# Optimization experiments

Hardware: AMD Instinct MI355X
Metric: run time of the kernel (lower is better)

Reference implementation:

```python
import jax, jax.numpy as jnp
import numpy as np
from jax import lax

M, B, D = 32, 64, 8192  # history length, batch of systems, degrees of freedom


def setup_inputs() -> dict:
    key = jax.random.key(0)
    k1, k2, k3 = jax.random.split(key, 3)
    s = jax.random.normal(k1, (M, B, D), dtype=jnp.float32)
    y = jax.random.normal(k2, (M, B, D), dtype=jnp.float32)
    frc = jax.random.normal(k3, (B, D), dtype=jnp.float32)
    return {"s": s, "y": y, "frc": frc}


def reference(s, y, frc):
    # r_i = 1 / (s_i . y_i), per batch row, as stored by extend()
    r = 1.0 / jnp.sum(s * y, axis=-1, keepdims=True)  # [M, B, 1]

    # First loop: iterate history from newest (i = M-1) to oldest (i = 0)
    def back_step(q, carry):
        si, yi, ri = carry
        ai = ri * jnp.sum(si * q, axis=-1, keepdims=True)  # [B, 1]
        q = q - ai * yi
        return q, ai

    q0 = -frc
    q, a_rev = lax.scan(back_step, q0, (s[::-1], y[::-1], r[::-1]))
    a = a_rev[::-1]  # a[i] now aligned with history index i

    # Initial Hessian scaling gamma = (s_last . y_last) / (y_last . y_last)
    g = (jnp.sum(s[-1] * y[-1], axis=-1) / jnp.sum(y[-1] * y[-1], axis=-1))[:, None]
    q = g * q

    # Second loop: oldest to newest
    def fwd_step(q, carry):
        si, yi, ri, ai = carry
        bi = ri * jnp.sum(yi * q, axis=-1, keepdims=True)
        q = q + si * (ai - bi)
        return q, None

    q, _ = lax.scan(fwd_step, q, (s, y, r, a))
    return -q
```

## Files before the change

### kernel.cpp

```cpp
#include <hip/hip_runtime.h>

#define Mh 32
#define Bh 64
#define Dh 8192
#define KCH 1024
#define NCH (Dh / KCH)
#define STG 128
#define NST (KCH / STG)

#define OFF_PSY 0
#define OFF_PYY 524288
#define OFF_PVS 1048576
#define OFF_PVY (OFF_PVS + 16384)
#define OFF_CY  (OFF_PVY + 16384)
#define OFF_CS  (OFF_CY + 2048)
#define OFF_G   (OFF_CS + 2048)

__global__ __launch_bounds__(256) void gram_kernel(
    const float* __restrict__ s, const float* __restrict__ y,
    const float* __restrict__ frc, float* __restrict__ ws)
{
    __shared__ float sT[32 * STG];
    __shared__ float yT[32 * STG];
    __shared__ float fT[STG];

    const int b  = blockIdx.x & 63;
    const int ch = blockIdx.x >> 6;
    const int k0 = ch * KCH;
    const int t  = threadIdx.x;
    const int w  = t >> 6;
    const int l  = t & 63;
    const int tx = l & 7;
    const int ty = l >> 3;
    const size_t base = (size_t)b * Dh;

    float asy[4][4] = {};
    float ayy[4][4] = {};
    float avs[4] = {}, avy[4] = {};

    int ri[4], rc[4];
    #pragma unroll
    for (int rep = 0; rep < 4; ++rep) {
        const int idx = t + rep * 256;
        ri[rep] = idx >> 5;
        rc[rep] = idx & 31;
    }

    float4 pS[4], pY[4], pF;
    auto issue = [&](int kb) {
        #pragma unroll
        for (int rep = 0; rep < 4; ++rep) {
            const size_t off = ((size_t)ri[rep] * Bh) * Dh + base + kb + (rc[rep] << 2);
            pS[rep] = *(const float4*)(s + off);
            pY[rep] = *(const float4*)(y + off);
        }
        if (t < 32) pF = *(const float4*)(frc + base + kb + (t << 2));
    };

    issue(k0);
    for (int st = 0; st < NST; ++st) {
        __syncthreads();
        #pragma unroll
        for (int rep = 0; rep < 4; ++rep) {
            const int col = rc[rep] ^ ((ri[rep] >> 2) & 7);
            *(float4*)&sT[ri[rep] * STG + (col << 2)] = pS[rep];
            *(float4*)&yT[ri[rep] * STG + (col << 2)] = pY[rep];
        }
        if (t < 32) *(float4*)&fT[t << 2] = pF;
        __syncthreads();
        if (st + 1 < NST) issue(k0 + (st + 1) * STG);

        #pragma unroll
        for (int kk = 0; kk < 8; ++kk) {
            const int c0 = (w << 3) + kk;
            float4 sv[4], tv[4], xv[4];
            #pragma unroll
            for (int aa = 0; aa < 4; ++aa) {
                sv[aa] = *(const float4*)&sT[((ty << 2) + aa) * STG + ((c0 ^ ty) << 2)];
                tv[aa] = *(const float4*)&yT[((ty << 2) + aa) * STG + ((c0 ^ ty) << 2)];
                xv[aa] = *(const float4*)&yT[((tx << 2) + aa) * STG + ((c0 ^ tx) << 2)];
            }
            const float4 fv = *(const float4*)&fT[c0 << 2];
            #pragma unroll
            for (int aa = 0; aa < 4; ++aa) {
                #pragma unroll
                for (int cc = 0; cc < 4; ++cc) {
                    asy[aa][cc] += sv[aa].x * xv[cc].x + sv[aa].y * xv[cc].y
                                 + sv[aa].z * xv[cc].z + sv[aa].w * xv[cc].w;
                    ayy[aa][cc] += tv[aa].x * xv[cc].x + tv[aa].y * xv[cc].y
                                 + tv[aa].z * xv[cc].z + tv[aa].w * xv[cc].w;
                }
                avs[aa] += sv[aa].x * fv.x + sv[aa].y * fv.y + sv[aa].z * fv.z + sv[aa].w * fv.w;
                avy[aa] += tv[aa].x * fv.x + tv[aa].y * fv.y + tv[aa].z * fv.z + tv[aa].w * fv.w;
            }
        }
    }

    __syncthreads();
    for (int wv = 0; wv < 4; ++wv) {
        if (w == wv) {
            #pragma unroll
            for (int aa = 0; aa < 4; ++aa) {
                #pragma unroll
                for (int cc = 0; cc < 4; ++cc) {
                    const int e = ((ty << 2) + aa) * 32 + (tx << 2) + cc;
                    if (wv == 0) { sT[e] = asy[aa][cc];  yT[e] = ayy[aa][cc]; }
                    else         { sT[e] += asy[aa][cc]; yT[e] += ayy[aa][cc]; }
                }
                if (tx == 0) {
                    const int i = (ty << 2) + aa;
                    if (wv == 0) { fT[i] = avs[aa];  fT[32 + i] = avy[aa]; }
                    else         { fT[i] += avs[aa]; fT[32 + i] += avy[aa]; }
                }
            }
        }
        __syncthreads();
    }

    float* PSY = ws + OFF_PSY + ((size_t)ch * Bh + b) * 1024;
    float* PYY = ws + OFF_PYY + ((size_t)ch * Bh + b) * 1024;
    *(float4*)&PSY[t << 2] = *(const float4*)&sT[t << 2];
    *(float4*)&PYY[t << 2] = *(const float4*)&yT[t << 2];
    if (t < 32)      ws[OFF_PVS + (ch * 64 + b) * 32 + t] = fT[t];
    else if (t < 64) ws[OFF_PVY + (ch * 64 + b) * 32 + (t - 32)] = fT[t];
}

__global__ __launch_bounds__(256) void recur_kernel(float* __restrict__ ws)
{
    __shared__ float WSY[1024], WYY[1024], VS[32], VY[32];
    const int b = blockIdx.x;
    const int t = threadIdx.x;

    float4 a4 = make_float4(0.f, 0.f, 0.f, 0.f);
    float4 c4 = make_float4(0.f, 0.f, 0.f, 0.f);
    #pragma unroll
    for (int ch = 0; ch < NCH; ++ch) {
        const float4 u = *(const float4*)&ws[OFF_PSY + ((size_t)ch * Bh + b) * 1024 + (t << 2)];
        const float4 v = *(const float4*)&ws[OFF_PYY + ((size_t)ch * Bh + b) * 1024 + (t << 2)];
        a4.x += u.x; a4.y += u.y; a4.z += u.z; a4.w += u.w;
        c4.x += v.x; c4.y += v.y; c4.z += v.z; c4.w += v.w;
    }
    *(float4*)&WSY[t << 2] = a4;
    *(float4*)&WYY[t << 2] = c4;
    if (t < 32) {
        float av = 0.f, cv = 0.f;
        #pragma unroll
        for (int ch = 0; ch < NCH; ++ch) {
            av += ws[OFF_PVS + (ch * 64 + b) * 32 + t];
            cv += ws[OFF_PVY + (ch * 64 + b) * 32 + t];
        }
        VS[t] = av; VY[t] = cv;
    }
    __syncthreads();
    if (t >= 64) return;

    const int i = t & 31;
    float row_sy[32], col_sy[32], row_yy[32];
    #pragma unroll
    for (int j = 0; j < 32; ++j) {
        row_sy[j] = WSY[i * 32 + j];
        col_sy[j] = WSY[j * 32 + i];
        row_yy[j] = WYY[i * 32 + j];
    }

    const double r = 1.0 / (double)row_sy[i];
    double acc = -(double)VS[i];
    double a_val = 0.0;
    #pragma unroll
    for (int j = 31; j >= 0; --j) {
        const double aj = __shfl(r, j) * __shfl(acc, j);
        if (i == j) a_val = aj;
        if (i < j)  acc -= aj * (double)row_sy[j];
    }

    const double g = (double)WSY[31 * 32 + 31] / (double)WYY[31 * 32 + 31];

    double u = -(double)VY[i];
    #pragma unroll
    for (int j = 0; j < 32; ++j)
        u -= __shfl(a_val, j) * (double)row_yy[j];
    u *= g;

    double tt = u;
    double b_val = 0.0;
    #pragma unroll
    for (int j = 0; j < 32; ++j) {
        const double bj = __shfl(r, j) * __shfl(tt, j);
        if (i == j) b_val = bj;
        const double dj = __shfl(a_val, j) - bj;
        if (i > j) tt += dj * (double)col_sy[j];
    }

    if (t < 32) {
        ws[OFF_CY + b * 32 + i] = (float)(g * a_val);
        ws[OFF_CS + b * 32 + i] = (float)(b_val - a_val);
    }
    if (t == 0) ws[OFF_G + b] = (float)g;
}

__global__ __launch_bounds__(256) void combine_kernel(
    const float* __restrict__ s, const float* __restrict__ y,
    const float* __restrict__ frc, const float* __restrict__ ws,
    float* __restrict__ out)
{
    __shared__ float cy[32], cs[32];
    const int b  = blockIdx.x & 63;
    const int ch = blockIdx.x >> 6;
    const int t  = threadIdx.x;
    if (t < 32) { cy[t] = ws[OFF_CY + b * 32 + t]; cs[t] = ws[OFF_CS + b * 32 + t]; }
    __syncthreads();

    const int d = ch * 1024 + (t << 2);
    const size_t base = (size_t)b * Dh + d;
    const float g = ws[OFF_G + b];
    const float4 fv = *(const float4*)(frc + base);
    float4 acc;
    acc.x = g * fv.x; acc.y = g * fv.y; acc.z = g * fv.z; acc.w = g * fv.w;

    const float* py = y + base;
    const float* ps = s + base;
    #pragma unroll
    for (int grp = 0; grp < 4; ++grp) {
        float4 yv[8], sv[8];
        #pragma unroll
        for (int j = 0; j < 8; ++j) {
            const size_t off = (size_t)(grp * 8 + j) * ((size_t)Bh * Dh);
            yv[j] = *(const float4*)(py + off);
            sv[j] = *(const float4*)(ps + off);
        }
        #pragma unroll
        for (int j = 0; j < 8; ++j) {
            const float a1 = cy[grp * 8 + j], a2 = cs[grp * 8 + j];
            acc.x += a1 * yv[j].x + a2 * sv[j].x;
            acc.y += a1 * yv[j].y + a2 * sv[j].y;
            acc.z += a1 * yv[j].z + a2 * sv[j].z;
            acc.w += a1 * yv[j].w + a2 * sv[j].w;
        }
    }
    *(float4*)(out + base) = acc;
}

extern "C" void kernel_launch(void* const* d_in, const int* in_sizes, int n_in,
                              void* d_out, int out_size, void* d_ws, size_t ws_size,
                              hipStream_t stream)
{
    const float* s   = (const float*)d_in[0];
    const float* y   = (const float*)d_in[1];
    const float* frc = (const float*)d_in[2];
    float* out = (float*)d_out;
    float* ws  = (float*)d_ws;

    gram_kernel<<<dim3(Bh * NCH), dim3(256), 0, stream>>>(s, y, frc, ws);
    recur_kernel<<<dim3(Bh), dim3(256), 0, stream>>>(ws);
    combine_kernel<<<dim3(Bh * NCH), dim3(256), 0, stream>>>(s, y, frc, ws, out);
}
```

Measured before the change: 255.7 us.

## Use async global-to-LDS loads in gram kernel and split combine into two passes

The gram kernel now streams s/y tiles directly into double-buffered LDS with global_load_lds and reads frc straight from global memory. The chunk count grows to 16 when the workspace allows, which doubles the number of gram blocks. The combine step optionally becomes two kernels: one writes per-history-row weighted rows to the workspace and another reduces them. That second path adds roughly 64MB of extra write and read traffic in exchange for more parallelism. Workspace offsets are now computed at runtime from ws_size.

```diff
diff --git a/kernel.cpp b/kernel.cpp
--- a/kernel.cpp
+++ b/kernel.cpp
@@ -3,92 +3,98 @@
 #define Mh 32
 #define Bh 64
 #define Dh 8192
-#define KCH 1024
-#define NCH (Dh / KCH)
 #define STG 128
-#define NST (KCH / STG)
-
-#define OFF_PSY 0
-#define OFF_PYY 524288
-#define OFF_PVS 1048576
-#define OFF_PVY (OFF_PVS + 16384)
-#define OFF_CY  (OFF_PVY + 16384)
-#define OFF_CS  (OFF_CY + 2048)
-#define OFF_G   (OFF_CS + 2048)
+
+typedef unsigned int u32;
+
+__device__ __forceinline__ void async_cp16(const float* g, float* l) {
+    __builtin_amdgcn_global_load_lds((const __attribute__((address_space(1))) u32*)g,
+                                     (__attribute__((address_space(3))) u32*)l, 16, 0, 0);
+}
 
 __global__ __launch_bounds__(256) void gram_kernel(
     const float* __restrict__ s, const float* __restrict__ y,
-    const float* __restrict__ frc, float* __restrict__ ws)
-{
-    __shared__ float sT[32 * STG];
-    __shared__ float yT[32 * STG];
-    __shared__ float fT[STG];
-
+    const float* __restrict__ frc, float* __restrict__ ws,
+    int nch, int kch,
+    long off_psy, long off_pyy, long off_pvs, long off_pvy)
+{
+    __shared__ float sT[2][32 * STG];
+    __shared__ float yT[2][32 * STG];
     const int b  = blockIdx.x & 63;
     const int ch = blockIdx.x >> 6;
-    const int k0 = ch * KCH;
+    const int k0 = ch * kch;
+    const int nst = kch / STG;
     const int t  = threadIdx.x;
     const int w  = t >> 6;
     const int l  = t & 63;
     const int tx = l & 7;
     const int ty = l >> 3;
-    const size_t base = (size_t)b * Dh;
-
-    float asy[4][4] = {};
-    float ayy[4][4] = {};
+
+    const float* sp[4]; const float* yp[4]; int lofs[4];
+    #pragma unroll
+    for (int jj = 0; jj < 4; ++jj) {
+        const int j   = (w << 2) + jj;
+        const int row = (j << 1) + (l >> 5);
+        const int cg  = (l & 31) ^ ((j >> 1) & 7);
+        const size_t goff = ((size_t)row * Bh + b) * Dh + k0 + (cg << 2);
+        sp[jj] = s + goff;
+        yp[jj] = y + goff;
+        lofs[jj] = j << 8;
+    }
+    const float* frcp = frc + (size_t)b * Dh + k0;
+
+    float acc_sy[4][4] = {};
+    float acc_yy[4][4] = {};
     float avs[4] = {}, avy[4] = {};
 
-    int ri[4], rc[4];
-    #pragma unroll
-    for (int rep = 0; rep < 4; ++rep) {
-        const int idx = t + rep * 256;
-        ri[rep] = idx >> 5;
-        rc[rep] = idx & 31;
-    }
-
-    float4 pS[4], pY[4], pF;
-    auto issue = [&](int kb) {
-        #pragma unroll
-        for (int rep = 0; rep < 4; ++rep) {
-            const size_t off = ((size_t)ri[rep] * Bh) * Dh + base + kb + (rc[rep] << 2);
-            pS[rep] = *(const float4*)(s + off);
-            pY[rep] = *(const float4*)(y + off);
-        }
-        if (t < 32) pF = *(const float4*)(frc + base + kb + (t << 2));
-    };
-
-    issue(k0);
-    for (int st = 0; st < NST; ++st) {
+    #pragma unroll
+    for (int jj = 0; jj < 4; ++jj) {
+        async_cp16(sp[jj], &sT[0][lofs[jj]]);
+        async_cp16(yp[jj], &yT[0][lofs[jj]]);
+        sp[jj] += STG; yp[jj] += STG;
+    }
+
+    for (int st = 0; st < nst; ++st) {
+        const int cur = st & 1;
         __syncthreads();
-        #pragma unroll
-        for (int rep = 0; rep < 4; ++rep) {
-            const int col = rc[rep] ^ ((ri[rep] >> 2) & 7);
-            *(float4*)&sT[ri[rep] * STG + (col << 2)] = pS[rep];
-            *(float4*)&yT[ri[rep] * STG + (col << 2)] = pY[rep];
-        }
-        if (t < 32) *(float4*)&fT[t << 2] = pF;
-        __syncthreads();
-        if (st + 1 < NST) issue(k0 + (st + 1) * STG);
-
+
+        float4 fvs[8];
+        #pragma unroll
+        for (int kk = 0; kk < 8; ++kk)
+            fvs[kk] = *(const float4*)(frcp + (((w << 3) + kk) << 2));
+        __builtin_amdgcn_sched_barrier(0);
+        frcp += STG;
+
+        if (st + 1 < nst) {
+            #pragma unroll
+            for (int jj = 0; jj < 4; ++jj) {
+                async_cp16(sp[jj], &sT[cur ^ 1][lofs[jj]]);
+                async_cp16(yp[jj], &yT[cur ^ 1][lofs[jj]]);
+                sp[jj] += STG; yp[jj] += STG;
+            }
+        }
+
+        const float* sb = sT[cur];
+        const float* yb = yT[cur];
         #pragma unroll
         for (int kk = 0; kk < 8; ++kk) {
             const int c0 = (w << 3) + kk;
             float4 sv[4], tv[4], xv[4];
             #pragma unroll
             for (int aa = 0; aa < 4; ++aa) {
-                sv[aa] = *(const float4*)&sT[((ty << 2) + aa) * STG + ((c0 ^ ty) << 2)];
-                tv[aa] = *(const float4*)&yT[((ty << 2) + aa) * STG + ((c0 ^ ty) << 2)];
-                xv[aa] = *(const float4*)&yT[((tx << 2) + aa) * STG + ((c0 ^ tx) << 2)];
+                sv[aa] = *(const float4*)&sb[((ty << 2) + aa) * STG + ((c0 ^ ty) << 2)];
+                tv[aa] = *(const float4*)&yb[((ty << 2) + aa) * STG + ((c0 ^ ty) << 2)];
+                xv[aa] = *(const float4*)&yb[((tx << 2) + aa) * STG + ((c0 ^ tx) << 2)];
             }
-            const float4 fv = *(const float4*)&fT[c0 << 2];
+            const float4 fv = fvs[kk];
             #pragma unroll
             for (int aa = 0; aa < 4; ++aa) {
                 #pragma unroll
                 for (int cc = 0; cc < 4; ++cc) {
-                    asy[aa][cc] += sv[aa].x * xv[cc].x + sv[aa].y * xv[cc].y
-                                 + sv[aa].z * xv[cc].z + sv[aa].w * xv[cc].w;
-                    ayy[aa][cc] += tv[aa].x * xv[cc].x + tv[aa].y * xv[cc].y
-                                 + tv[aa].z * xv[cc].z + tv[aa].w * xv[cc].w;
+                    acc_sy[aa][cc] += sv[aa].x * xv[cc].x + sv[aa].y * xv[cc].y
+                                    + sv[aa].z * xv[cc].z + sv[aa].w * xv[cc].w;
+                    acc_yy[aa][cc] += tv[aa].x * xv[cc].x + tv[aa].y * xv[cc].y
+                                    + tv[aa].z * xv[cc].z + tv[aa].w * xv[cc].w;
                 }
                 avs[aa] += sv[aa].x * fv.x + sv[aa].y * fv.y + sv[aa].z * fv.z + sv[aa].w * fv.w;
                 avy[aa] += tv[aa].x * fv.x + tv[aa].y * fv.y + tv[aa].z * fv.z + tv[aa].w * fv.w;
@@ -97,6 +103,9 @@
     }
 
     __syncthreads();
+    float* SY = &sT[0][0];
+    float* YY = &sT[1][0];
+    float* VV = &yT[0][0];
     for (int wv = 0; wv < 4; ++wv) {
         if (w == wv) {
             #pragma unroll
@@ -104,28 +113,31 @@
                 #pragma unroll
                 for (int cc = 0; cc < 4; ++cc) {
                     const int e = ((ty << 2) + aa) * 32 + (tx << 2) + cc;
-                    if (wv == 0) { sT[e] = asy[aa][cc];  yT[e] = ayy[aa][cc]; }
-                    else         { sT[e] += asy[aa][cc]; yT[e] += ayy[aa][cc]; }
+                    if (wv == 0) { SY[e] = acc_sy[aa][cc];  YY[e] = acc_yy[aa][cc]; }
+                    else         { SY[e] += acc_sy[aa][cc]; YY[e] += acc_yy[aa][cc]; }
                 }
                 if (tx == 0) {
                     const int i = (ty << 2) + aa;
-                    if (wv == 0) { fT[i] = avs[aa];  fT[32 + i] = avy[aa]; }
-                    else         { fT[i] += avs[aa]; fT[32 + i] += avy[aa]; }
+                    if (wv == 0) { VV[i] = avs[aa];  VV[32 + i] = avy[aa]; }
+                    else         { VV[i] += avs[aa]; VV[32 + i] += avy[aa]; }
                 }
             }
         }
         __syncthreads();
     }
 
-    float* PSY = ws + OFF_PSY + ((size_t)ch * Bh + b) * 1024;
-    float* PYY = ws + OFF_PYY + ((size_t)ch * Bh + b) * 1024;
-    *(float4*)&PSY[t << 2] = *(const float4*)&sT[t << 2];
-    *(float4*)&PYY[t << 2] = *(const float4*)&yT[t << 2];
-    if (t < 32)      ws[OFF_PVS + (ch * 64 + b) * 32 + t] = fT[t];
-    else if (t < 64) ws[OFF_PVY + (ch * 64 + b) * 32 + (t - 32)] = fT[t];
-}
-
-__global__ __launch_bounds__(256) void recur_kernel(float* __restrict__ ws)
+    float* PSY = ws + off_psy + ((size_t)ch * Bh + b) * 1024;
+    float* PYY = ws + off_pyy + ((size_t)ch * Bh + b) * 1024;
+    *(float4*)&PSY[t << 2] = *(const float4*)&SY[t << 2];
+    *(float4*)&PYY[t << 2] = *(const float4*)&YY[t << 2];
+    if (t < 32)      ws[off_pvs + (ch * 64 + b) * 32 + t] = VV[t];
+    else if (t < 64) ws[off_pvy + (ch * 64 + b) * 32 + (t - 32)] = VV[t];
+}
+
+__global__ __launch_bounds__(256) void recur_kernel(
+    float* __restrict__ ws, int nch,
+    long off_psy, long off_pyy, long off_pvs, long off_pvy,
+    long off_cy, long off_cs, long off_g)
 {
     __shared__ float WSY[1024], WYY[1024], VS[32], VY[32];
     const int b = blockIdx.x;
@@ -133,10 +145,9 @@
 
     float4 a4 = make_float4(0.f, 0.f, 0.f, 0.f);
     float4 c4 = make_float4(0.f, 0.f, 0.f, 0.f);
-    #pragma unroll
-    for (int ch = 0; ch < NCH; ++ch) {
-        const float4 u = *(const float4*)&ws[OFF_PSY + ((size_t)ch * Bh + b) * 1024 + (t << 2)];
-        const float4 v = *(const float4*)&ws[OFF_PYY + ((size_t)ch * Bh + b) * 1024 + (t << 2)];
+    for (int ch = 0; ch < nch; ++ch) {
+        const float4 u = *(const float4*)&ws[off_psy + ((size_t)ch * Bh + b) * 1024 + (t << 2)];
+        const float4 v = *(const float4*)&ws[off_pyy + ((size_t)ch * Bh + b) * 1024 + (t << 2)];
         a4.x += u.x; a4.y += u.y; a4.z += u.z; a4.w += u.w;
         c4.x += v.x; c4.y += v.y; c4.z += v.z; c4.w += v.w;
     }
@@ -144,10 +155,9 @@
     *(float4*)&WYY[t << 2] = c4;
     if (t < 32) {
         float av = 0.f, cv = 0.f;
-        #pragma unroll
-        for (int ch = 0; ch < NCH; ++ch) {
-            av += ws[OFF_PVS + (ch * 64 + b) * 32 + t];
-            cv += ws[OFF_PVY + (ch * 64 + b) * 32 + t];
+        for (int ch = 0; ch < nch; ++ch) {
+            av += ws[off_pvs + (ch * 64 + b) * 32 + t];
+            cv += ws[off_pvy + (ch * 64 + b) * 32 + t];
         }
         VS[t] = av; VY[t] = cv;
     }
@@ -192,27 +202,81 @@
     }
 
     if (t < 32) {
-        ws[OFF_CY + b * 32 + i] = (float)(g * a_val);
-        ws[OFF_CS + b * 32 + i] = (float)(b_val - a_val);
-    }
-    if (t == 0) ws[OFF_G + b] = (float)g;
+        ws[off_cy + b * 32 + i] = (float)(g * a_val);
+        ws[off_cs + b * 32 + i] = (float)(b_val - a_val);
+    }
+    if (t == 0) ws[off_g + b] = (float)g;
+}
+
+__global__ __launch_bounds__(256) void wrow_kernel(
+    const float* __restrict__ s, const float* __restrict__ y,
+    const float* __restrict__ ws, float* __restrict__ part_ws,
+    long off_cy, long off_cs, long off_part)
+{
+    const int b = blockIdx.x & 63;
+    const int i = blockIdx.x >> 6;
+    const int t = threadIdx.x;
+    const float a1 = ws[off_cy + (b << 5) + i];
+    const float a2 = ws[off_cs + (b << 5) + i];
+    const float* ys = y + ((size_t)i * Bh + b) * Dh;
+    const float* ss = s + ((size_t)i * Bh + b) * Dh;
+    float* pd = part_ws + off_part + ((size_t)b * Mh + i) * Dh;
+    #pragma unroll
+    for (int rep = 0; rep < 8; ++rep) {
+        const int d = (rep << 10) + (t << 2);
+        const float4 yv = *(const float4*)(ys + d);
+        const float4 sv = *(const float4*)(ss + d);
+        float4 o;
+        o.x = a1 * yv.x + a2 * sv.x;
+        o.y = a1 * yv.y + a2 * sv.y;
+        o.z = a1 * yv.z + a2 * sv.z;
+        o.w = a1 * yv.w + a2 * sv.w;
+        *(float4*)(pd + d) = o;
+    }
+}
+
+__global__ __launch_bounds__(256) void finish_kernel(
+    const float* __restrict__ frc, const float* __restrict__ ws,
+    float* __restrict__ out, long off_g, long off_part)
+{
+    const int b  = blockIdx.x & 63;
+    const int ch = blockIdx.x >> 6;
+    const int t  = threadIdx.x;
+    const int d  = (ch << 10) + (t << 2);
+    const float g = ws[off_g + b];
+    const float4 fv = *(const float4*)(frc + (size_t)b * Dh + d);
+    float4 acc;
+    acc.x = g * fv.x; acc.y = g * fv.y; acc.z = g * fv.z; acc.w = g * fv.w;
+    const float* p = ws + off_part + ((size_t)b * Mh) * Dh + d;
+    #pragma unroll
+    for (int grp = 0; grp < 4; ++grp) {
+        float4 v[8];
+        #pragma unroll
+        for (int j = 0; j < 8; ++j)
+            v[j] = *(const float4*)(p + (size_t)(grp * 8 + j) * Dh);
+        #pragma unroll
+        for (int j = 0; j < 8; ++j) {
+            acc.x += v[j].x; acc.y += v[j].y; acc.z += v[j].z; acc.w += v[j].w;
+        }
+    }
+    *(float4*)(out + (size_t)b * Dh + d) = acc;
 }
 
 __global__ __launch_bounds__(256) void combine_kernel(
     const float* __restrict__ s, const float* __restrict__ y,
     const float* __restrict__ frc, const float* __restrict__ ws,
-    float* __restrict__ out)
+    float* __restrict__ out, long off_cy, long off_cs, long off_g)
 {
     __shared__ float cy[32], cs[32];
     const int b  = blockIdx.x & 63;
     const int ch = blockIdx.x >> 6;
     const int t  = threadIdx.x;
-    if (t < 32) { cy[t] = ws[OFF_CY + b * 32 + t]; cs[t] = ws[OFF_CS + b * 32 + t]; }
+    if (t < 32) { cy[t] = ws[off_cy + b * 32 + t]; cs[t] = ws[off_cs + b * 32 + t]; }
     __syncthreads();
 
     const int d = ch * 1024 + (t << 2);
     const size_t base = (size_t)b * Dh + d;
-    const float g = ws[OFF_G + b];
+    const float g = ws[off_g + b];
     const float4 fv = *(const float4*)(frc + base);
     float4 acc;
     acc.x = g * fv.x; acc.y = g * fv.y; acc.z = g * fv.z; acc.w = g * fv.w;
@@ -250,7 +314,36 @@
     float* out = (float*)d_out;
     float* ws  = (float*)d_ws;
 
-    gram_kernel<<<dim3(Bh * NCH), dim3(256), 0, stream>>>(s, y, frc, ws);
-    recur_kernel<<<dim3(Bh), dim3(256), 0, stream>>>(ws);
-    combine_kernel<<<dim3(Bh * NCH), dim3(256), 0, stream>>>(s, y, frc, ws, out);
-}
+    const long floats = (long)(ws_size / 4);
+
+    int nch = 16;
+    long P, off_psy, off_pyy, off_pvs, off_pvy, off_cy, off_cs, off_g, endc;
+    for (int attempt = 0; attempt < 2; ++attempt) {
+        P = (long)nch * 64 * 1024;
+        off_psy = 0; off_pyy = P; off_pvs = 2 * P;
+        off_pvy = off_pvs + (long)nch * 64 * 32;
+        off_cy  = off_pvy + (long)nch * 64 * 32;
+        off_cs  = off_cy + 2048;
+        off_g   = off_cs + 2048;
+        endc    = off_g + 64;
+        if (endc <= floats || nch == 8) break;
+        nch = 8;
+    }
+    const long off_part = (endc + 3) & ~3L;
+    const bool two_pass = (off_part + (long)Bh * Mh * Dh) <= floats;
+    const int kch = Dh / nch;
+
+    gram_kernel<<<dim3(Bh * nch), dim3(256), 0, stream>>>(
+        s, y, frc, ws, nch, kch, off_psy, off_pyy, off_pvs, off_pvy);
+    recur_kernel<<<dim3(Bh), dim3(256), 0, stream>>>(
+        ws, nch, off_psy, off_pyy, off_pvs, off_pvy, off_cy, off_cs, off_g);
+    if (two_pass) {
+        wrow_kernel<<<dim3(Bh * Mh), dim3(256), 0, stream>>>(
+            s, y, ws, ws, off_cy, off_cs, off_part);
+        finish_kernel<<<dim3(Bh * 8), dim3(256), 0, stream>>>(
+            frc, ws, out, off_g, off_part);
+    } else {
+        combine_kernel<<<dim3(Bh * 8), dim3(256), 0, stream>>>(
+            s, y, frc, ws, out, off_cy, off_cs, off_g);
+    }
+}
```

New measurement: 321.3 us. +25.7%, slower.

## Split gram and combine passes across more blocks with staggered chunks

Applied to the files above, without the earlier changes.

The gram kernel now uses 16 K-chunks of 512 instead of 8 chunks of 1024, with a smaller 64-wide staging tile and no register prefetch. Chunk order is rotated by batch index to spread memory traffic. The combine step is split across the history dimension into two partial kernels whose results are summed in a final kernel. This raises block count and occupancy in exchange for extra workspace traffic, an extra kernel launch, and the loss of software prefetch overlap in the gram loop.

```diff
diff --git a/kernel.cpp b/kernel.cpp
--- a/kernel.cpp
+++ b/kernel.cpp
@@ -3,18 +3,19 @@
 #define Mh 32
 #define Bh 64
 #define Dh 8192
-#define KCH 1024
-#define NCH (Dh / KCH)
-#define STG 128
+#define NCHG 16
+#define KCH 512
+#define STG 64
 #define NST (KCH / STG)
 
-#define OFF_PSY 0
-#define OFF_PYY 524288
-#define OFF_PVS 1048576
-#define OFF_PVY (OFF_PVS + 16384)
-#define OFF_CY  (OFF_PVY + 16384)
-#define OFF_CS  (OFF_CY + 2048)
-#define OFF_G   (OFF_CS + 2048)
+#define OFF_PSY 0L
+#define OFF_PYY 1048576L
+#define OFF_PVS 2097152L
+#define OFF_PVY 2129920L
+#define OFF_CY  2162688L
+#define OFF_CS  2164736L
+#define OFF_G   2166784L
+#define OFF_PC  2166848L
 
 __global__ __launch_bounds__(256) void gram_kernel(
     const float* __restrict__ s, const float* __restrict__ y,
@@ -24,79 +25,77 @@
     __shared__ float yT[32 * STG];
     __shared__ float fT[STG];
 
-    const int b  = blockIdx.x & 63;
-    const int ch = blockIdx.x >> 6;
-    const int k0 = ch * KCH;
-    const int t  = threadIdx.x;
-    const int w  = t >> 6;
-    const int l  = t & 63;
-    const int tx = l & 7;
-    const int ty = l >> 3;
-    const size_t base = (size_t)b * Dh;
+    const int b   = blockIdx.x & 63;
+    const int ch  = blockIdx.x >> 6;
+    const int chk = (ch + b) & 15;
+    const int k0  = chk * KCH;
+    const int t   = threadIdx.x;
+    const int w   = t >> 6;
+    const int l   = t & 63;
+    const int tx  = l & 7;
+    const int ty  = l >> 3;
+
+    size_t go[2]; int la[2];
+    #pragma unroll
+    for (int r = 0; r < 2; ++r) {
+        const int row = (t + (r << 8)) >> 4;
+        const int cl  = t & 15;
+        const int gc  = cl ^ (row >> 2);
+        go[r] = ((size_t)row * Bh + b) * Dh + (gc << 2);
+        la[r] = (row << 6) + (cl << 2);
+    }
+    const size_t fb = (size_t)b * Dh;
 
     float asy[4][4] = {};
     float ayy[4][4] = {};
     float avs[4] = {}, avy[4] = {};
 
-    int ri[4], rc[4];
-    #pragma unroll
-    for (int rep = 0; rep < 4; ++rep) {
-        const int idx = t + rep * 256;
-        ri[rep] = idx >> 5;
-        rc[rep] = idx & 31;
-    }
-
-    float4 pS[4], pY[4], pF;
-    auto issue = [&](int kb) {
+    for (int st = 0; st < NST; ++st) {
+        const int k = k0 + st * STG;
+        const float4 s0 = *(const float4*)(s + go[0] + k);
+        const float4 y0 = *(const float4*)(y + go[0] + k);
+        const float4 s1 = *(const float4*)(s + go[1] + k);
+        const float4 y1 = *(const float4*)(y + go[1] + k);
+        float4 fv4 = make_float4(0.f, 0.f, 0.f, 0.f);
+        if (t < 16) fv4 = *(const float4*)(frc + fb + k + (t << 2));
+
+        __syncthreads();
+        *(float4*)&sT[la[0]] = s0;
+        *(float4*)&yT[la[0]] = y0;
+        *(float4*)&sT[la[1]] = s1;
+        *(float4*)&yT[la[1]] = y1;
+        if (t < 16) *(float4*)&fT[t << 2] = fv4;
+        __syncthreads();
+
         #pragma unroll
-        for (int rep = 0; rep < 4; ++rep) {
-            const size_t off = ((size_t)ri[rep] * Bh) * Dh + base + kb + (rc[rep] << 2);
-            pS[rep] = *(const float4*)(s + off);
-            pY[rep] = *(const float4*)(y + off);
-        }
-        if (t < 32) pF = *(const float4*)(frc + base + kb + (t << 2));
-    };
-
-    issue(k0);
-    for (int st = 0; st < NST; ++st) {
-        __syncthreads();
-        #pragma unroll
-        for (int rep = 0; rep < 4; ++rep) {
-            const int col = rc[rep] ^ ((ri[rep] >> 2) & 7);
-            *(float4*)&sT[ri[rep] * STG + (col << 2)] = pS[rep];
-            *(float4*)&yT[ri[rep] * STG + (col << 2)] = pY[rep];
-        }
-        if (t < 32) *(float4*)&fT[t << 2] = pF;
-        __syncthreads();
-        if (st + 1 < NST) issue(k0 + (st + 1) * STG);
-
-        #pragma unroll
-        for (int kk = 0; kk < 8; ++kk) {
-            const int c0 = (w << 3) + kk;
-            float4 sv[4], tv[4], xv[4];
+        for (int kk = 0; kk < 4; ++kk) {
+            const int c0 = (w << 2) + kk;
+            float4 xv[4];
             #pragma unroll
-            for (int aa = 0; aa < 4; ++aa) {
-                sv[aa] = *(const float4*)&sT[((ty << 2) + aa) * STG + ((c0 ^ ty) << 2)];
-                tv[aa] = *(const float4*)&yT[((ty << 2) + aa) * STG + ((c0 ^ ty) << 2)];
-                xv[aa] = *(const float4*)&yT[((tx << 2) + aa) * STG + ((c0 ^ tx) << 2)];
-            }
+            for (int aa = 0; aa < 4; ++aa)
+                xv[aa] = *(const float4*)&yT[(((tx << 2) + aa) << 6) + ((c0 ^ tx) << 2)];
             const float4 fv = *(const float4*)&fT[c0 << 2];
             #pragma unroll
             for (int aa = 0; aa < 4; ++aa) {
+                const float4 sv = *(const float4*)&sT[(((ty << 2) + aa) << 6) + ((c0 ^ ty) << 2)];
+                const float4 tv = *(const float4*)&yT[(((ty << 2) + aa) << 6) + ((c0 ^ ty) << 2)];
                 #pragma unroll
                 for (int cc = 0; cc < 4; ++cc) {
-                    asy[aa][cc] += sv[aa].x * xv[cc].x + sv[aa].y * xv[cc].y
-                                 + sv[aa].z * xv[cc].z + sv[aa].w * xv[cc].w;
-                    ayy[aa][cc] += tv[aa].x * xv[cc].x + tv[aa].y * xv[cc].y
-                                 + tv[aa].z * xv[cc].z + tv[aa].w * xv[cc].w;
+                    asy[aa][cc] += sv.x * xv[cc].x + sv.y * xv[cc].y
+                                 + sv.z * xv[cc].z + sv.w * xv[cc].w;
+                    ayy[aa][cc] += tv.x * xv[cc].x + tv.y * xv[cc].y
+                                 + tv.z * xv[cc].z + tv.w * xv[cc].w;
                 }
-                avs[aa] += sv[aa].x * fv.x + sv[aa].y * fv.y + sv[aa].z * fv.z + sv[aa].w * fv.w;
-                avy[aa] += tv[aa].x * fv.x + tv[aa].y * fv.y + tv[aa].z * fv.z + tv[aa].w * fv.w;
+                avs[aa] += sv.x * fv.x + sv.y * fv.y + sv.z * fv.z + sv.w * fv.w;
+                avy[aa] += tv.x * fv.x + tv.y * fv.y + tv.z * fv.z + tv.w * fv.w;
             }
         }
     }
 
     __syncthreads();
+    float* SY = &sT[0];
+    float* YY = &sT[1024];
+    float* VV = &fT[0];
     for (int wv = 0; wv < 4; ++wv) {
         if (w == wv) {
             #pragma unroll
@@ -104,13 +103,13 @@
                 #pragma unroll
                 for (int cc = 0; cc < 4; ++cc) {
                     const int e = ((ty << 2) + aa) * 32 + (tx << 2) + cc;
-                    if (wv == 0) { sT[e] = asy[aa][cc];  yT[e] = ayy[aa][cc]; }
-                    else         { sT[e] += asy[aa][cc]; yT[e] += ayy[aa][cc]; }
+                    if (wv == 0) { SY[e] = asy[aa][cc];  YY[e] = ayy[aa][cc]; }
+                    else         { SY[e] += asy[aa][cc]; YY[e] += ayy[aa][cc]; }
                 }
                 if (tx == 0) {
                     const int i = (ty << 2) + aa;
-                    if (wv == 0) { fT[i] = avs[aa];  fT[32 + i] = avy[aa]; }
-                    else         { fT[i] += avs[aa]; fT[32 + i] += avy[aa]; }
+                    if (wv == 0) { VV[i] = avs[aa];  VV[32 + i] = avy[aa]; }
+                    else         { VV[i] += avs[aa]; VV[32 + i] += avy[aa]; }
                 }
             }
         }
@@ -119,10 +118,10 @@
 
     float* PSY = ws + OFF_PSY + ((size_t)ch * Bh + b) * 1024;
     float* PYY = ws + OFF_PYY + ((size_t)ch * Bh + b) * 1024;
-    *(float4*)&PSY[t << 2] = *(const float4*)&sT[t << 2];
-    *(float4*)&PYY[t << 2] = *(const float4*)&yT[t << 2];
-    if (t < 32)      ws[OFF_PVS + (ch * 64 + b) * 32 + t] = fT[t];
-    else if (t < 64) ws[OFF_PVY + (ch * 64 + b) * 32 + (t - 32)] = fT[t];
+    *(float4*)&PSY[t << 2] = *(const float4*)&SY[t << 2];
+    *(float4*)&PYY[t << 2] = *(const float4*)&YY[t << 2];
+    if (t < 32)      ws[OFF_PVS + (ch * 64 + b) * 32 + t] = VV[t];
+    else if (t < 64) ws[OFF_PVY + (ch * 64 + b) * 32 + (t - 32)] = VV[t];
 }
 
 __global__ __launch_bounds__(256) void recur_kernel(float* __restrict__ ws)
@@ -133,8 +132,7 @@
 
     float4 a4 = make_float4(0.f, 0.f, 0.f, 0.f);
     float4 c4 = make_float4(0.f, 0.f, 0.f, 0.f);
-    #pragma unroll
-    for (int ch = 0; ch < NCH; ++ch) {
+    for (int ch = 0; ch < NCHG; ++ch) {
         const float4 u = *(const float4*)&ws[OFF_PSY + ((size_t)ch * Bh + b) * 1024 + (t << 2)];
         const float4 v = *(const float4*)&ws[OFF_PYY + ((size_t)ch * Bh + b) * 1024 + (t << 2)];
         a4.x += u.x; a4.y += u.y; a4.z += u.z; a4.w += u.w;
@@ -144,8 +142,7 @@
     *(float4*)&WYY[t << 2] = c4;
     if (t < 32) {
         float av = 0.f, cv = 0.f;
-        #pragma unroll
-        for (int ch = 0; ch < NCH; ++ch) {
+        for (int ch = 0; ch < NCHG; ++ch) {
             av += ws[OFF_PVS + (ch * 64 + b) * 32 + t];
             cv += ws[OFF_PVY + (ch * 64 + b) * 32 + t];
         }
@@ -198,46 +195,66 @@
     if (t == 0) ws[OFF_G + b] = (float)g;
 }
 
-__global__ __launch_bounds__(256) void combine_kernel(
+__global__ __launch_bounds__(256) void combine_part(
     const float* __restrict__ s, const float* __restrict__ y,
-    const float* __restrict__ frc, const float* __restrict__ ws,
-    float* __restrict__ out)
-{
-    __shared__ float cy[32], cs[32];
+    const float* __restrict__ ws, float* __restrict__ pc)
+{
+    __shared__ float cy[16], cs[16];
     const int b  = blockIdx.x & 63;
-    const int ch = blockIdx.x >> 6;
+    const int ch = (blockIdx.x >> 6) & 7;
+    const int h  = blockIdx.x >> 9;
     const int t  = threadIdx.x;
-    if (t < 32) { cy[t] = ws[OFF_CY + b * 32 + t]; cs[t] = ws[OFF_CS + b * 32 + t]; }
+    if (t < 16) {
+        cy[t] = ws[OFF_CY + (b << 5) + (h << 4) + t];
+        cs[t] = ws[OFF_CS + (b << 5) + (h << 4) + t];
+    }
     __syncthreads();
 
-    const int d = ch * 1024 + (t << 2);
+    const int d = (ch << 10) + (t << 2);
     const size_t base = (size_t)b * Dh + d;
-    const float g = ws[OFF_G + b];
-    const float4 fv = *(const float4*)(frc + base);
-    float4 acc;
-    acc.x = g * fv.x; acc.y = g * fv.y; acc.z = g * fv.z; acc.w = g * fv.w;
-
-    const float* py = y + base;
-    const float* ps = s + base;
-    #pragma unroll
-    for (int grp = 0; grp < 4; ++grp) {
+    float4 acc = make_float4(0.f, 0.f, 0.f, 0.f);
+
+    #pragma unroll
+    for (int grp = 0; grp < 2; ++grp) {
         float4 yv[8], sv[8];
         #pragma unroll
         for (int j = 0; j < 8; ++j) {
-            const size_t off = (size_t)(grp * 8 + j) * ((size_t)Bh * Dh);
-            yv[j] = *(const float4*)(py + off);
-            sv[j] = *(const float4*)(ps + off);
+            const int i = (h << 4) + (grp << 3) + j;
+            const size_t off = base + (size_t)i * ((size_t)Bh * Dh);
+            yv[j] = *(const float4*)(y + off);
+            sv[j] = *(const float4*)(s + off);
         }
         #pragma unroll
         for (int j = 0; j < 8; ++j) {
-            const float a1 = cy[grp * 8 + j], a2 = cs[grp * 8 + j];
+            const float a1 = cy[(grp << 3) + j], a2 = cs[(grp << 3) + j];
             acc.x += a1 * yv[j].x + a2 * sv[j].x;
             acc.y += a1 * yv[j].y + a2 * sv[j].y;
             acc.z += a1 * yv[j].z + a2 * sv[j].z;
             acc.w += a1 * yv[j].w + a2 * sv[j].w;
         }
     }
-    *(float4*)(out + base) = acc;
+    *(float4*)(pc + ((size_t)h * Bh * Dh) + base) = acc;
+}
+
+__global__ __launch_bounds__(256) void combine_fin(
+    const float* __restrict__ frc, const float* __restrict__ ws,
+    const float* __restrict__ pc, float* __restrict__ out)
+{
+    const int b  = blockIdx.x & 63;
+    const int ch = blockIdx.x >> 6;
+    const int t  = threadIdx.x;
+    const int d  = (ch << 10) + (t << 2);
+    const size_t base = (size_t)b * Dh + d;
+    const float g = ws[OFF_G + b];
+    const float4 fv = *(const float4*)(frc + base);
+    const float4 p0 = *(const float4*)(pc + base);
+    const float4 p1 = *(const float4*)(pc + (size_t)Bh * Dh + base);
+    float4 o;
+    o.x = g * fv.x + p0.x + p1.x;
+    o.y = g * fv.y + p0.y + p1.y;
+    o.z = g * fv.z + p0.z + p1.z;
+    o.w = g * fv.w + p0.w + p1.w;
+    *(float4*)(out + base) = o;
 }
 
 extern "C" void kernel_launch(void* const* d_in, const int* in_sizes, int n_in,
@@ -249,8 +266,10 @@
     const float* frc = (const float*)d_in[2];
     float* out = (float*)d_out;
     float* ws  = (float*)d_ws;
-
-    gram_kernel<<<dim3(Bh * NCH), dim3(256), 0, stream>>>(s, y, frc, ws);
+    float* pc  = ws + OFF_PC;
+
+    gram_kernel<<<dim3(Bh * NCHG), dim3(256), 0, stream>>>(s, y, frc, ws);
     recur_kernel<<<dim3(Bh), dim3(256), 0, stream>>>(ws);
-    combine_kernel<<<dim3(Bh * NCH), dim3(256), 0, stream>>>(s, y, frc, ws, out);
-}
+    combine_part<<<dim3(Bh * 8 * 2), dim3(256), 0, stream>>>(s, y, ws, pc);
+    combine_fin<<<dim3(Bh * 8), dim3(256), 0, stream>>>(frc, ws, pc, out);
+}
```

After: 234.3 us. 1.09x faster.
